# Kernel tuning notes

Hardware: AMD Instinct MI355X
Metric: run time of the kernel (lower is better)

## Reference

```python
import jax, jax.numpy as jnp
import numpy as np

EPS = 1e-8


def _autocorr2d(x):
    # x: [B, H, W] single-channel batch
    B, H, W = x.shape
    xc = x - x.mean(axis=(-2, -1), keepdims=True)
    # torch.std defaults to unbiased (ddof=1)
    xn = xc / (xc.std(axis=(-2, -1), ddof=1, keepdims=True) + EPS)
    ph, pw = H // 4, W // 4
    # grouped cross-correlation: input [1,B,H,W], kernel [B,1,H,W], groups=B
    # (lax conv, like torch conv2d, does NOT flip the kernel)
    corr = jax.lax.conv_general_dilated(
        xn[None],            # [1, B, H, W]
        xn[:, None],         # [B, 1, H, W]
        window_strides=(1, 1),
        padding=((ph, ph), (pw, pw)),
        feature_group_count=B,
        dimension_numbers=('NCHW', 'OIHW', 'NCHW'),
    )  # [1, B, 2*(H//4)+1, 2*(W//4)+1]
    norm = jnp.sqrt(jnp.sum(xn ** 2, axis=(-2, -1))).reshape(B, 1, 1, 1)
    # Faithful to the original: [1,B,oh,ow] / [B,1,1,1] broadcasts to [B,B,oh,ow]
    # (the torch .squeeze(0) is a no-op on the resulting shape)
    return corr / (norm + EPS)


def _channel_mean_corr(x):
    # x: [B, C, H, W] -> mean over channels of per-channel autocorr -> [B, B, oh, ow]
    return jax.vmap(_autocorr2d, in_axes=1)(x).mean(axis=0)


def setup_inputs() -> dict:
    key = jax.random.key(0)
    k1, k2 = jax.random.split(key)
    B, C, H, W = 8, 3, 192, 192
    pred = jax.random.normal(k1, (B, C, H, W), dtype=jnp.float32)
    target = jax.random.normal(k2, (B, C, H, W), dtype=jnp.float32)
    return {"pred": pred, "target": target}


def reference(pred, target):
    pred_corr = _channel_mean_corr(pred)
    target_corr = _channel_mean_corr(target)
    pred_corr = pred_corr / (pred_corr.max() + EPS)
    target_corr = target_corr / (target_corr.max() + EPS)
    return jnp.mean(jnp.abs(pred_corr - target_corr))
```

## Files before the change

kernel.cpp:

```cpp
#include <hip/hip_runtime.h>
#include <math.h>

#define EPSF 1e-8f
#define HW 36864
#define SHALF 4753

#define OFF_INV    0
#define OFF_NORM   48
#define OFF_MAX    144
#define OFF_ACC    146
#define OFF_CNT3   148
#define OFF_PART   160
#define OFF_CTR    256
#define OFF_PARTS  1024
#define OFF_SRED   3651328
#define OFF_PREP   3879472

#define CY 12
#define AR 61
#define APITCH 400
#define CPB4 736
#define RBW (4*CPB4)
#define ABYTES (AR*APITCH)
#define BBYTES (4*2*RBW)
#define LDSB (ABYTES + BBYTES)
#define ESTR 240

#define RSEG 19
#define RCHK 251
#define LOSSB2 38

typedef short short8 __attribute__((ext_vector_type(8)));
typedef float f32x4 __attribute__((ext_vector_type(4)));

__device__ __forceinline__ unsigned int pk2(float a, float b) {
  union { float f; unsigned int u; } x, y;
  x.f = a; y.f = b;
  unsigned int ra = x.u + 0x7fffu + ((x.u >> 16) & 1u);
  unsigned int rb = y.u + 0x7fffu + ((y.u >> 16) & 1u);
  return (ra >> 16) | (rb & 0xffff0000u);
}

__global__ __launch_bounds__(256) void stats_prep(const float* __restrict__ pred,
                                                  const float* __restrict__ target,
                                                  float* __restrict__ ws) {
  int blk = blockIdx.x, tid = threadIdx.x;
  int img = blk >> 2, qtr = blk & 3;
  int t = img / 24, local = img % 24;
  const float* src = (t ? target : pred) + (size_t)local * HW + qtr * 9216;

  const float4* s4 = (const float4*)src;
  float s = 0.f, sq = 0.f;
  for (int i = tid; i < 2304; i += 256) {
    float4 v = s4[i];
    s  += (v.x + v.y) + (v.z + v.w);
    sq += (v.x*v.x + v.y*v.y) + (v.z*v.z + v.w*v.w);
  }
#pragma unroll
  for (int o = 32; o > 0; o >>= 1) { s += __shfl_down(s, o); sq += __shfl_down(sq, o); }
  __shared__ float rs[4], rq[4], bcast[1];
  int lane = tid & 63, wv = tid >> 6;
  if (!lane) { rs[wv] = s; rq[wv] = sq; }
  __syncthreads();
  if (!tid) {
    s  = (rs[0] + rs[1]) + (rs[2] + rs[3]);
    sq = (rq[0] + rq[1]) + (rq[2] + rq[3]);
    atomicAdd(&ws[OFF_PART + 2*img],     s);
    atomicAdd(&ws[OFF_PART + 2*img + 1], sq);
    __threadfence();
    atomicAdd((int*)ws + OFF_CTR + img, 1);
    while (atomicAdd((int*)ws + OFF_CTR + img, 0) < 4) { }
    float S1 = atomicAdd(&ws[OFF_PART + 2*img],     0.f);
    float Q  = atomicAdd(&ws[OFF_PART + 2*img + 1], 0.f);
    float mean = S1 / (float)HW;
    float M2 = fmaxf(Q - S1 * S1 / (float)HW, 0.f);
    float inv = 1.f / (sqrtf(M2 / (float)(HW - 1)) + EPSF);
    bcast[0] = mean;
    if (qtr == 0) {
      ws[OFF_INV  + img] = inv;
      ws[OFF_NORM + img] = sqrtf(M2) * inv;
    }
  }
  __syncthreads();
  float mean = bcast[0];
  unsigned short* prep = (unsigned short*)(ws + OFF_PREP) + (size_t)img * HW + qtr * 9216;
  for (int i = tid; i < 2304; i += 256) {
    float4 v = s4[i];
    uint2 d; d.x = pk2(v.x - mean, v.y - mean); d.y = pk2(v.z - mean, v.w - mean);
    *(uint2*)(prep + i * 4) = d;
  }
}

__device__ __forceinline__ void writeB4(char* buf, uint4 qA, uint4 qB, int lane) {
  if (lane < 45) {
    unsigned int D[6];
    D[0] = qA.x; D[1] = qA.y; D[2] = qA.z; D[3] = qA.w; D[4] = qB.x; D[5] = qB.y;
    unsigned int Sh[5];
#pragma unroll
    for (int j = 0; j < 5; j++) Sh[j] = (D[j] >> 16) | (D[j+1] << 16);
    char* base = buf + lane * 16;
    uint4 v0; v0.x = D[0];  v0.y = D[1];  v0.z = D[2];  v0.w = D[3];
    uint4 v1; v1.x = Sh[0]; v1.y = Sh[1]; v1.z = Sh[2]; v1.w = Sh[3];
    uint4 v2; v2.x = D[1];  v2.y = D[2];  v2.z = D[3];  v2.w = D[4];
    uint4 v3; v3.x = Sh[1]; v3.y = Sh[2]; v3.z = Sh[3]; v3.w = Sh[4];
    *(uint4*)(base)            = v0;
    *(uint4*)(base + CPB4)     = v1;
    *(uint4*)(base + 2*CPB4)   = v2;
    *(uint4*)(base + 3*CPB4)   = v3;
  }
}

__global__ __launch_bounds__(256, 3) void autocorr_mfma(float* __restrict__ ws) {
  int blk = blockIdx.x;
  int img = blk >> 4, chunk = blk & 15;
  int Y = chunk * CY;
  const unsigned short* prep = (const unsigned short*)(ws + OFF_PREP) + (size_t)img * HW;
  float inv = ws[OFF_INV + img];
  float scale = inv * inv;

  __shared__ __align__(16) char lds[LDSB];
  char* Al = lds;
  char* Bl = lds + ABYTES;

  int tid = threadIdx.x;
  int w = tid >> 6, lane = tid & 63, c = lane & 15, h = lane >> 4;
  int rw = w & 1, sh = w >> 1;

  int p8 = (8 - (c & 7)) & 7;
  int p4 = p8 & 3;
  int q_l = (c == 0) ? 0 : ((c <= 8) ? 1 : 2);
  int LB0 = p4 * CPB4 + 16 * (h - q_l) + 128 + ((p8 & 4) ? 8 : 0);

  char* myB = Bl + w * (2 * RBW);

  uint4 qA, qB;
  qA.x = qA.y = qA.z = qA.w = 0u; qB.x = qB.y = qB.z = qB.w = 0u;
  {
    const char* rowp = (const char*)(prep + (Y + rw) * 192) + lane * 16 - 224;
    if (lane >= 14 && lane <= 37) qA = *(const uint4*)rowp;
    if (lane >= 13 && lane <= 36) qB = *(const uint4*)(rowp + 16);
  }

  int RV = 192 - Y;
  for (int m = tid; m < AR * 24; m += 256) {
    int r = m / 24, k = m - r * 24;
    short8 v = (short8)(short)0;
    if (r < RV) v = *(const short8*)(prep + (Y + r) * 192 + k * 8);
    *(short8*)(Al + r * APITCH + k * 16) = v;
  }

  writeB4(myB, qA, qB, lane);
  __syncthreads();

  f32x4 acc[2][7];
#pragma unroll
  for (int mtl = 0; mtl < 2; mtl++)
#pragma unroll
    for (int nt = 0; nt < 7; nt++) acc[mtl][nt] = (f32x4)0.f;

  union WU { uint2 u2[2]; short8 s8; };

#pragma unroll 1
  for (int k = 0; k < 6; k++) {
    uint4 nA, nB;
    nA.x = nA.y = nA.z = nA.w = 0u; nB.x = nB.y = nB.z = nB.w = 0u;
    if (k < 5) {
      const char* rowp = (const char*)(prep + (Y + 2*(k+1) + rw) * 192) + lane * 16 - 224;
      if (lane >= 14 && lane <= 37) nA = *(const uint4*)rowp;
      if (lane >= 13 && lane <= 36) nB = *(const uint4*)(rowp + 16);
    }

    const char* pB = myB + (k & 1) * RBW + LB0;
    int i = 2 * k + rw;
    int rb0, rb1;
    {
      int ra0 = i + 16 * (2 * sh) + c;
      int ra1 = ra0 + 16;
      rb0 = (ra0 > 60 ? 60 : ra0) * APITCH + 16 * h;
      rb1 = (ra1 > 60 ? 60 : ra1) * APITCH + 16 * h;
    }

    short8 Wf[8];
#pragma unroll
    for (int wi = 0; wi < 7; wi++) {
      WU u; u.u2[0] = *(const uint2*)(pB + 32 * wi); u.u2[1] = *(const uint2*)(pB + 32 * wi + 8);
      Wf[wi] = u.s8;
    }
#pragma unroll
    for (int t = 0; t < 6; t++) {
      short8 A0 = *(const short8*)(Al + rb0 + 64 * t);
      short8 A1 = *(const short8*)(Al + rb1 + 64 * t);
      __builtin_amdgcn_s_setprio(1);
#pragma unroll
      for (int nt = 0; nt < 7; nt++)
        acc[0][nt] = __builtin_amdgcn_mfma_f32_16x16x32_bf16(A0, Wf[(2*t+6-nt) & 7], acc[0][nt], 0, 0, 0);
#pragma unroll
      for (int nt = 0; nt < 7; nt++)
        acc[1][nt] = __builtin_amdgcn_mfma_f32_16x16x32_bf16(A1, Wf[(2*t+6-nt) & 7], acc[1][nt], 0, 0, 0);
      __builtin_amdgcn_s_setprio(0);
      if (t < 5) {
        WU ua; ua.u2[0] = *(const uint2*)(pB + 32*(2*t+7)); ua.u2[1] = *(const uint2*)(pB + 32*(2*t+7) + 8);
        Wf[(2*t+7) & 7] = ua.s8;
        WU ub; ub.u2[0] = *(const uint2*)(pB + 32*(2*t+8)); ub.u2[1] = *(const uint2*)(pB + 32*(2*t+8) + 8);
        Wf[(2*t+8) & 7] = ub.s8;
      }
    }
    if (k < 5) writeB4(myB + ((k + 1) & 1) * RBW, nA, nB, lane);
  }

  __syncthreads();
  if (rw == 1) {
    char* rg = lds + sh * (64 * ESTR) + lane * ESTR;
#pragma unroll
    for (int mtl = 0; mtl < 2; mtl++)
#pragma unroll
      for (int nt = 0; nt < 7; nt++) *(f32x4*)(rg + (mtl*7+nt)*16) = acc[mtl][nt];
  }
  __syncthreads();
  if (rw == 0) {
    const char* rg = lds + sh * (64 * ESTR) + lane * ESTR;
    float* part = ws + OFF_PARTS + (size_t)blk * SHALF;
#pragma unroll
    for (int mtl = 0; mtl < 2; mtl++) {
#pragma unroll
      for (int nt = 0; nt < 7; nt++) {
        f32x4 o = *(const f32x4*)(rg + (mtl*7+nt)*16);
        int s = 16 * nt + c;
        if (s <= 96) {
#pragma unroll
          for (int r = 0; r < 4; r++) {
            int sy = 16 * (2 * sh + mtl) + 4 * h + r;
            if (sy <= 48)
              part[sy * 97 + s] = (acc[mtl][nt][r] + o[r]) * scale;
          }
        }
      }
    }
  }
}

__global__ __launch_bounds__(256) void reduce_max(float* __restrict__ ws) {
  int blk = blockIdx.x;
  int tj = blk / RSEG, seg = blk - tj * RSEG;
  int t = tj >> 3, jb = tj & 7;
  int imgbase = t * 24 + jb * 3;
  int tid = threadIdx.x;
  __shared__ float wsh[24];
  if (tid < 24) wsh[tid] = (1.f / 3.f) / (ws[OFF_NORM + t * 24 + tid] + EPSF);
  __syncthreads();
  int off = seg * RCHK + tid;
  bool act = (tid < RCHK) && (off < SHALF);
  float p0 = 0.f, p1 = 0.f, p2 = 0.f;
  if (act) {
    const float* P = ws + OFF_PARTS;
    const float* pa = P + (size_t)((imgbase + 0) * 16) * SHALF + off;
    const float* pb = P + (size_t)((imgbase + 1) * 16) * SHALF + off;
    const float* pc = P + (size_t)((imgbase + 2) * 16) * SHALF + off;
#pragma unroll
    for (int ch = 0; ch < 16; ch++) {
      p0 += pa[ch * SHALF]; p1 += pb[ch * SHALF]; p2 += pc[ch * SHALF];
    }
    float* Sred = ws + OFF_SRED;
    Sred[(size_t)(imgbase + 0) * SHALF + off] = p0;
    Sred[(size_t)(imgbase + 1) * SHALF + off] = p1;
    Sred[(size_t)(imgbase + 2) * SHALF + off] = p2;
  }
  float mx = 0.f;
#pragma unroll
  for (int i = 0; i < 8; i++)
    mx = fmaxf(mx, p0 * wsh[i*3] + p1 * wsh[i*3+1] + p2 * wsh[i*3+2]);
#pragma unroll
  for (int o = 32; o > 0; o >>= 1) mx = fmaxf(mx, __shfl_down(mx, o));
  __shared__ float rp[4];
  int lane = tid & 63, wv = tid >> 6;
  if (!lane) rp[wv] = mx;
  __syncthreads();
  if (!tid) {
    mx = fmaxf(fmaxf(rp[0], rp[1]), fmaxf(rp[2], rp[3]));
    atomicMax((int*)ws + OFF_MAX + t, __float_as_int(mx));
  }
}

__global__ __launch_bounds__(256) void loss_final(float* __restrict__ ws,
                                                  float* __restrict__ out) {
  __shared__ float wsh[48];
  int tid = threadIdx.x;
  if (tid < 48) wsh[tid] = (1.f / 3.f) / (ws[OFF_NORM + tid] + EPSF);
  __syncthreads();
  float imp = 1.f / (__int_as_float(((const int*)ws)[OFF_MAX])     + EPSF);
  float imt = 1.f / (__int_as_float(((const int*)ws)[OFF_MAX + 1]) + EPSF);
  float acc = 0.f;
  const float* Sred = ws + OFF_SRED;
  for (int idx = blockIdx.x * 256 + tid; idx < 8 * SHALF; idx += LOSSB2 * 256) {
    int jb = idx / SHALF, off = idx - jb * SHALF;
    const float* Pp = Sred + (size_t)(3 * jb) * SHALF + off;
    const float* Tt = Sred + (size_t)(24 + 3 * jb) * SHALF + off;
    float p0 = Pp[0], p1 = Pp[SHALF], p2 = Pp[2 * SHALF];
    float q0 = Tt[0], q1 = Tt[SHALF], q2 = Tt[2 * SHALF];
    float a8 = 0.f;
#pragma unroll
    for (int i = 0; i < 8; i++) {
      float pv = (p0 * wsh[i*3] + p1 * wsh[i*3+1] + p2 * wsh[i*3+2]) * imp;
      float tv = (q0 * wsh[24+i*3] + q1 * wsh[24+i*3+1] + q2 * wsh[24+i*3+2]) * imt;
      a8 += fabsf(pv - tv);
    }
    acc += ((off < 97) ? 1.f : 2.f) * a8;
  }
#pragma unroll
  for (int o = 32; o > 0; o >>= 1) acc += __shfl_down(acc, o);
  __shared__ float r[4];
  int lane = tid & 63, wv = tid >> 6;
  if (!lane) r[wv] = acc;
  __syncthreads();
  if (!tid) {
    float bs = (r[0] + r[1]) + (r[2] + r[3]);
    atomicAdd(&ws[OFF_ACC], bs);
    __threadfence();
    int old = atomicAdd((int*)ws + OFF_CNT3, 1);
    if (old == LOSSB2 - 1) {
      float total = atomicAdd(&ws[OFF_ACC], 0.f);
      out[0] = total * (1.0f / 602176.0f);
    }
  }
}

extern "C" void kernel_launch(void* const* d_in, const int* in_sizes, int n_in,
                              void* d_out, int out_size, void* d_ws, size_t ws_size,
                              hipStream_t stream) {
  const float* pred   = (const float*)d_in[0];
  const float* target = (const float*)d_in[1];
  float* ws  = (float*)d_ws;
  float* out = (float*)d_out;

  hipMemsetAsync((char*)d_ws + 144 * sizeof(float), 0, 160 * sizeof(float), stream);
  hipLaunchKernelGGL(stats_prep,    dim3(192),       dim3(256), 0, stream, pred, target, ws);
  hipLaunchKernelGGL(autocorr_mfma, dim3(768),       dim3(256), 0, stream, ws);
  hipLaunchKernelGGL(reduce_max,    dim3(16 * RSEG), dim3(256), 0, stream, ws);
  hipLaunchKernelGGL(loss_final,    dim3(LOSSB2),    dim3(256), 0, stream, ws, out);
}
```

Before: 61.43 us.

## Fuse partial reduction and max into autocorr kernel via last-block counters

Removes the separate reduce_max kernel launch. In autocorr_mfma, the last of the 16 chunk blocks for each image, detected through an atomic counter, sums the 16 partial correlation planes into Sred. The last image of each three-channel group then computes the weighted max and applies an atomicMax. This saves one kernel launch and its global round trip, but the tail reduction now runs serially in only a few blocks (48 and then 16) instead of 304 parallel blocks, and it adds threadfence and atomic overhead.

New measurement: 153.7 us. +150.3%, slower.

```diff
diff --git a/kernel.cpp b/kernel.cpp
--- a/kernel.cpp
+++ b/kernel.cpp
@@ -12,6 +12,8 @@
 #define OFF_CNT3   148
 #define OFF_PART   160
 #define OFF_CTR    256
+#define OFF_ICTR   304
+#define OFF_GCTR   352
 #define OFF_PARTS  1024
 #define OFF_SRED   3651328
 #define OFF_PREP   3879472
@@ -26,8 +28,6 @@
 #define LDSB (ABYTES + BBYTES)
 #define ESTR 240
 
-#define RSEG 19
-#define RCHK 251
 #define LOSSB2 38
 
 typedef short short8 __attribute__((ext_vector_type(8)));
@@ -119,6 +119,7 @@
   float scale = inv * inv;
 
   __shared__ __align__(16) char lds[LDSB];
+  __shared__ int sflag[2];
   char* Al = lds;
   char* Bl = lds + ABYTES;
 
@@ -237,47 +238,56 @@
       }
     }
   }
-}
-
-__global__ __launch_bounds__(256) void reduce_max(float* __restrict__ ws) {
-  int blk = blockIdx.x;
-  int tj = blk / RSEG, seg = blk - tj * RSEG;
-  int t = tj >> 3, jb = tj & 7;
-  int imgbase = t * 24 + jb * 3;
-  int tid = threadIdx.x;
-  __shared__ float wsh[24];
-  if (tid < 24) wsh[tid] = (1.f / 3.f) / (ws[OFF_NORM + t * 24 + tid] + EPSF);
-  __syncthreads();
-  int off = seg * RCHK + tid;
-  bool act = (tid < RCHK) && (off < SHALF);
-  float p0 = 0.f, p1 = 0.f, p2 = 0.f;
-  if (act) {
-    const float* P = ws + OFF_PARTS;
-    const float* pa = P + (size_t)((imgbase + 0) * 16) * SHALF + off;
-    const float* pb = P + (size_t)((imgbase + 1) * 16) * SHALF + off;
-    const float* pc = P + (size_t)((imgbase + 2) * 16) * SHALF + off;
-#pragma unroll
-    for (int ch = 0; ch < 16; ch++) {
-      p0 += pa[ch * SHALF]; p1 += pb[ch * SHALF]; p2 += pc[ch * SHALF];
-    }
-    float* Sred = ws + OFF_SRED;
-    Sred[(size_t)(imgbase + 0) * SHALF + off] = p0;
-    Sred[(size_t)(imgbase + 1) * SHALF + off] = p1;
-    Sred[(size_t)(imgbase + 2) * SHALF + off] = p2;
-  }
-  float mx = 0.f;
-#pragma unroll
-  for (int i = 0; i < 8; i++)
-    mx = fmaxf(mx, p0 * wsh[i*3] + p1 * wsh[i*3+1] + p2 * wsh[i*3+2]);
-#pragma unroll
-  for (int o = 32; o > 0; o >>= 1) mx = fmaxf(mx, __shfl_down(mx, o));
-  __shared__ float rp[4];
-  int lane = tid & 63, wv = tid >> 6;
-  if (!lane) rp[wv] = mx;
-  __syncthreads();
-  if (!tid) {
-    mx = fmaxf(fmaxf(rp[0], rp[1]), fmaxf(rp[2], rp[3]));
-    atomicMax((int*)ws + OFF_MAX + t, __float_as_int(mx));
+
+  __syncthreads();
+  if (tid == 0) {
+    __threadfence();
+    int done = atomicAdd((int*)ws + OFF_ICTR + img, 1);
+    sflag[0] = (done == 15) ? 1 : 0;
+  }
+  __syncthreads();
+  if (sflag[0]) {
+    __threadfence();
+    const float* P = ws + OFF_PARTS + (size_t)img * 16 * SHALF;
+    float* Sred = ws + OFF_SRED + (size_t)img * SHALF;
+    for (int off = tid; off < SHALF; off += 256) {
+      float s = 0.f;
+#pragma unroll
+      for (int ch = 0; ch < 16; ch++) s += P[ch * SHALF + off];
+      Sred[off] = s;
+    }
+    __syncthreads();
+    if (tid == 0) {
+      __threadfence();
+      int gdone = atomicAdd((int*)ws + OFF_GCTR + (img / 3), 1);
+      sflag[1] = (gdone == 2) ? 1 : 0;
+    }
+    __syncthreads();
+    if (sflag[1]) {
+      __threadfence();
+      int grp = img / 3;
+      int t = grp >> 3;
+      float* wshf = (float*)lds;
+      float* rmax = (float*)(lds + 128);
+      if (tid < 24) wshf[tid] = (1.f / 3.f) / (ws[OFF_NORM + t * 24 + tid] + EPSF);
+      __syncthreads();
+      const float* S0 = ws + OFF_SRED + (size_t)(grp * 3) * SHALF;
+      float mx = 0.f;
+      for (int off = tid; off < SHALF; off += 256) {
+        float p0 = S0[off], p1 = S0[SHALF + off], p2 = S0[2 * SHALF + off];
+#pragma unroll
+        for (int i = 0; i < 8; i++)
+          mx = fmaxf(mx, p0 * wshf[i*3] + p1 * wshf[i*3+1] + p2 * wshf[i*3+2]);
+      }
+#pragma unroll
+      for (int o = 32; o > 0; o >>= 1) mx = fmaxf(mx, __shfl_down(mx, o));
+      if (!(tid & 63)) rmax[tid >> 6] = mx;
+      __syncthreads();
+      if (!tid) {
+        mx = fmaxf(fmaxf(rmax[0], rmax[1]), fmaxf(rmax[2], rmax[3]));
+        atomicMax((int*)ws + OFF_MAX + t, __float_as_int(mx));
+      }
+    }
   }
 }
 
@@ -332,9 +342,8 @@
   float* ws  = (float*)d_ws;
   float* out = (float*)d_out;
 
-  hipMemsetAsync((char*)d_ws + 144 * sizeof(float), 0, 160 * sizeof(float), stream);
-  hipLaunchKernelGGL(stats_prep,    dim3(192),       dim3(256), 0, stream, pred, target, ws);
-  hipLaunchKernelGGL(autocorr_mfma, dim3(768),       dim3(256), 0, stream, ws);
-  hipLaunchKernelGGL(reduce_max,    dim3(16 * RSEG), dim3(256), 0, stream, ws);
-  hipLaunchKernelGGL(loss_final,    dim3(LOSSB2),    dim3(256), 0, stream, ws, out);
-}
+  hipMemsetAsync((char*)d_ws + 144 * sizeof(float), 0, (368 - 144) * sizeof(float), stream);
+  hipLaunchKernelGGL(stats_prep,    dim3(192),    dim3(256), 0, stream, pred, target, ws);
+  hipLaunchKernelGGL(autocorr_mfma, dim3(768),    dim3(256), 0, stream, ws);
+  hipLaunchKernelGGL(loss_final,    dim3(LOSSB2), dim3(256), 0, stream, ws, out);
+}
```

## Compute correlation max analytically from zero-lag energy and drop reduce_max kernel

Applied to the files above, without the earlier changes.

The global max of each channel-mean correlation map is now computed in stats_prep's last block from the zero-lag value, the sum of squares of the bf16-rounded centred data, instead of scanning every lag. This removes the separate reduce_max kernel and its Sred round trip, and loss_final now sums the 16 chunk partials directly with more blocks. It relies on the zero-lag entry always being the max, which holds for autocorrelation only if the normalisation never lets an off-diagonal batch pair exceed it. It also adds a last-block-done counter pattern in stats_prep.

Measured after the change: 84.97 us. +38.3%, slower.

```diff
diff --git a/kernel.cpp b/kernel.cpp
--- a/kernel.cpp
+++ b/kernel.cpp
@@ -5,15 +5,14 @@
 #define HW 36864
 #define SHALF 4753
 
-#define OFF_INV    0
-#define OFF_NORM   48
 #define OFF_MAX    144
 #define OFF_ACC    146
 #define OFF_CNT3   148
-#define OFF_PART   160
-#define OFF_CTR    256
+#define OFF_FCTR   150
+#define OFF_Q2     152
+#define OFF_PART   200
+#define OFF_CTR    296
 #define OFF_PARTS  1024
-#define OFF_SRED   3651328
 #define OFF_PREP   3879472
 
 #define CY 12
@@ -26,9 +25,7 @@
 #define LDSB (ABYTES + BBYTES)
 #define ESTR 240
 
-#define RSEG 19
-#define RCHK 251
-#define LOSSB2 38
+#define LOSSB2 64
 
 typedef short short8 __attribute__((ext_vector_type(8)));
 typedef float f32x4 __attribute__((ext_vector_type(4)));
@@ -59,6 +56,7 @@
 #pragma unroll
   for (int o = 32; o > 0; o >>= 1) { s += __shfl_down(s, o); sq += __shfl_down(sq, o); }
   __shared__ float rs[4], rq[4], bcast[1];
+  __shared__ int lastFlag;
   int lane = tid & 63, wv = tid >> 6;
   if (!lane) { rs[wv] = s; rq[wv] = sq; }
   __syncthreads();
@@ -77,17 +75,52 @@
     float inv = 1.f / (sqrtf(M2 / (float)(HW - 1)) + EPSF);
     bcast[0] = mean;
     if (qtr == 0) {
-      ws[OFF_INV  + img] = inv;
-      ws[OFF_NORM + img] = sqrtf(M2) * inv;
+      ws[img] = inv;
+      ws[48 + img] = sqrtf(M2) * inv;
     }
   }
   __syncthreads();
   float mean = bcast[0];
   unsigned short* prep = (unsigned short*)(ws + OFF_PREP) + (size_t)img * HW + qtr * 9216;
+  float sq2 = 0.f;
   for (int i = tid; i < 2304; i += 256) {
     float4 v = s4[i];
     uint2 d; d.x = pk2(v.x - mean, v.y - mean); d.y = pk2(v.z - mean, v.w - mean);
     *(uint2*)(prep + i * 4) = d;
+    float b0 = __uint_as_float(d.x << 16), b1 = __uint_as_float(d.x & 0xffff0000u);
+    float b2 = __uint_as_float(d.y << 16), b3 = __uint_as_float(d.y & 0xffff0000u);
+    sq2 += (b0*b0 + b1*b1) + (b2*b2 + b3*b3);
+  }
+#pragma unroll
+  for (int o = 32; o > 0; o >>= 1) sq2 += __shfl_down(sq2, o);
+  if (!lane) rs[wv] = sq2;
+  __syncthreads();
+  if (!tid) {
+    atomicAdd(&ws[OFF_Q2 + img], (rs[0] + rs[1]) + (rs[2] + rs[3]));
+    __threadfence();
+    int v = atomicAdd((int*)ws + OFF_FCTR, 1);
+    lastFlag = (v == 191) ? 1 : 0;
+  }
+  __syncthreads();
+  if (lastFlag) {
+    __threadfence();
+    float mx = 0.f;
+    if (tid < 128) {
+      int tt = tid >> 6, pair = tid & 63;
+      int ib = pair >> 3, bb = pair & 7;
+      float val = 0.f;
+#pragma unroll
+      for (int cc = 0; cc < 3; cc++) {
+        float q2  = ws[OFF_Q2 + tt*24 + bb*3 + cc];
+        float iv  = ws[tt*24 + bb*3 + cc];
+        float nrm = ws[48 + tt*24 + ib*3 + cc];
+        val += q2 * iv * iv / (nrm + EPSF);
+      }
+      mx = val * (1.f / 3.f);
+    }
+#pragma unroll
+    for (int o = 32; o > 0; o >>= 1) mx = fmaxf(mx, __shfl_down(mx, o));
+    if (tid < 128 && !lane) ws[OFF_MAX + (tid >> 6)] = mx;
   }
 }
 
@@ -115,7 +148,7 @@
   int img = blk >> 4, chunk = blk & 15;
   int Y = chunk * CY;
   const unsigned short* prep = (const unsigned short*)(ws + OFF_PREP) + (size_t)img * HW;
-  float inv = ws[OFF_INV + img];
+  float inv = ws[img];
   float scale = inv * inv;
 
   __shared__ __align__(16) char lds[LDSB];
@@ -239,64 +272,26 @@
   }
 }
 
-__global__ __launch_bounds__(256) void reduce_max(float* __restrict__ ws) {
-  int blk = blockIdx.x;
-  int tj = blk / RSEG, seg = blk - tj * RSEG;
-  int t = tj >> 3, jb = tj & 7;
-  int imgbase = t * 24 + jb * 3;
-  int tid = threadIdx.x;
-  __shared__ float wsh[24];
-  if (tid < 24) wsh[tid] = (1.f / 3.f) / (ws[OFF_NORM + t * 24 + tid] + EPSF);
-  __syncthreads();
-  int off = seg * RCHK + tid;
-  bool act = (tid < RCHK) && (off < SHALF);
-  float p0 = 0.f, p1 = 0.f, p2 = 0.f;
-  if (act) {
-    const float* P = ws + OFF_PARTS;
-    const float* pa = P + (size_t)((imgbase + 0) * 16) * SHALF + off;
-    const float* pb = P + (size_t)((imgbase + 1) * 16) * SHALF + off;
-    const float* pc = P + (size_t)((imgbase + 2) * 16) * SHALF + off;
-#pragma unroll
-    for (int ch = 0; ch < 16; ch++) {
-      p0 += pa[ch * SHALF]; p1 += pb[ch * SHALF]; p2 += pc[ch * SHALF];
-    }
-    float* Sred = ws + OFF_SRED;
-    Sred[(size_t)(imgbase + 0) * SHALF + off] = p0;
-    Sred[(size_t)(imgbase + 1) * SHALF + off] = p1;
-    Sred[(size_t)(imgbase + 2) * SHALF + off] = p2;
-  }
-  float mx = 0.f;
-#pragma unroll
-  for (int i = 0; i < 8; i++)
-    mx = fmaxf(mx, p0 * wsh[i*3] + p1 * wsh[i*3+1] + p2 * wsh[i*3+2]);
-#pragma unroll
-  for (int o = 32; o > 0; o >>= 1) mx = fmaxf(mx, __shfl_down(mx, o));
-  __shared__ float rp[4];
-  int lane = tid & 63, wv = tid >> 6;
-  if (!lane) rp[wv] = mx;
-  __syncthreads();
-  if (!tid) {
-    mx = fmaxf(fmaxf(rp[0], rp[1]), fmaxf(rp[2], rp[3]));
-    atomicMax((int*)ws + OFF_MAX + t, __float_as_int(mx));
-  }
-}
-
 __global__ __launch_bounds__(256) void loss_final(float* __restrict__ ws,
                                                   float* __restrict__ out) {
   __shared__ float wsh[48];
   int tid = threadIdx.x;
-  if (tid < 48) wsh[tid] = (1.f / 3.f) / (ws[OFF_NORM + tid] + EPSF);
-  __syncthreads();
-  float imp = 1.f / (__int_as_float(((const int*)ws)[OFF_MAX])     + EPSF);
-  float imt = 1.f / (__int_as_float(((const int*)ws)[OFF_MAX + 1]) + EPSF);
+  if (tid < 48) wsh[tid] = (1.f / 3.f) / (ws[48 + tid] + EPSF);
+  __syncthreads();
+  float imp = 1.f / (ws[OFF_MAX]     + EPSF);
+  float imt = 1.f / (ws[OFF_MAX + 1] + EPSF);
   float acc = 0.f;
-  const float* Sred = ws + OFF_SRED;
+  const float* P = ws + OFF_PARTS;
   for (int idx = blockIdx.x * 256 + tid; idx < 8 * SHALF; idx += LOSSB2 * 256) {
     int jb = idx / SHALF, off = idx - jb * SHALF;
-    const float* Pp = Sred + (size_t)(3 * jb) * SHALF + off;
-    const float* Tt = Sred + (size_t)(24 + 3 * jb) * SHALF + off;
-    float p0 = Pp[0], p1 = Pp[SHALF], p2 = Pp[2 * SHALF];
-    float q0 = Tt[0], q1 = Tt[SHALF], q2 = Tt[2 * SHALF];
+    const float* pb = P + (size_t)(3 * jb) * 16 * SHALF + off;
+    const float* tb = P + (size_t)((24 + 3 * jb) * 16) * SHALF + off;
+    float p0 = 0.f, p1 = 0.f, p2 = 0.f, q0 = 0.f, q1 = 0.f, q2 = 0.f;
+#pragma unroll
+    for (int ch = 0; ch < 16; ch++) {
+      p0 += pb[ch * SHALF]; p1 += pb[(16 + ch) * SHALF]; p2 += pb[(32 + ch) * SHALF];
+      q0 += tb[ch * SHALF]; q1 += tb[(16 + ch) * SHALF]; q2 += tb[(32 + ch) * SHALF];
+    }
     float a8 = 0.f;
 #pragma unroll
     for (int i = 0; i < 8; i++) {
@@ -332,9 +327,8 @@
   float* ws  = (float*)d_ws;
   float* out = (float*)d_out;
 
-  hipMemsetAsync((char*)d_ws + 144 * sizeof(float), 0, 160 * sizeof(float), stream);
-  hipLaunchKernelGGL(stats_prep,    dim3(192),       dim3(256), 0, stream, pred, target, ws);
-  hipLaunchKernelGGL(autocorr_mfma, dim3(768),       dim3(256), 0, stream, ws);
-  hipLaunchKernelGGL(reduce_max,    dim3(16 * RSEG), dim3(256), 0, stream, ws);
-  hipLaunchKernelGGL(loss_final,    dim3(LOSSB2),    dim3(256), 0, stream, ws, out);
-}
+  hipMemsetAsync((char*)d_ws + 144 * sizeof(float), 0, (352 - 144) * sizeof(float), stream);
+  hipLaunchKernelGGL(stats_prep,    dim3(192),    dim3(256), 0, stream, pred, target, ws);
+  hipLaunchKernelGGL(autocorr_mfma, dim3(768),    dim3(256), 0, stream, ws);
+  hipLaunchKernelGGL(loss_final,    dim3(LOSSB2), dim3(256), 0, stream, ws, out);
+}
```
